# Kernel tuning notes

Measured on AMD Instinct MI355X. Metric: run time of the kernel, lower is better.

Reference implementation:

```python
import jax, jax.numpy as jnp
import numpy as np

N, E, D, H, OUT, L, AH = 50000, 800000, 128, 128, 2, 4, 16
LN_EPS = 1e-5


def setup_inputs() -> dict:
    key = jax.random.key(0)
    ks = jax.random.split(key, 8)
    s = lambda k, shape, scale: jax.random.normal(k, shape, jnp.float32) * scale
    return {
        "node_features": jax.random.normal(ks[0], (N, D), jnp.float32),
        "edge_index": jax.random.randint(ks[1], (2, E), 0, N),
        "W_self": s(ks[2], (L, D, H), 0.05),
        "b_self": jnp.zeros((L, H), jnp.float32),
        "W_ctx": s(ks[3], (L, 2 * D, H), 0.05),
        "b_ctx": jnp.zeros((L, H), jnp.float32),
        "att_W1": s(ks[4], (L, H, AH), 0.1),
        "att_b1": jnp.zeros((L, AH), jnp.float32),
        "att_w2": s(ks[5], (L, AH), 0.1),
        "ln_gamma": jnp.ones((L, H), jnp.float32),
        "ln_beta": jnp.zeros((L, H), jnp.float32),
        "fusion_logits": jnp.ones((L,), jnp.float32),
        "cls_W": s(ks[6], (H, OUT), 0.05),
        "cls_b": jnp.zeros((OUT,), jnp.float32),
    }


def _aggregate(x, src, tgt, n):
    # PyG add-aggregation of message cat([x_i - x_j, x_j]) at target nodes.
    # sum_over_edges(x_tgt - x_src) at tgt == deg(tgt)*x[tgt] - sum x_src, so we
    # avoid materializing the [E, 2D] edge tensor.
    ones = jnp.ones((src.shape[0],), x.dtype)
    deg = jax.ops.segment_sum(ones, tgt, num_segments=n)          # [N]
    agg_j = jax.ops.segment_sum(x[src], tgt, num_segments=n)      # [N, D]
    return jnp.concatenate([deg[:, None] * x - agg_j, agg_j], -1)  # [N, 2D]


def _layer_norm(x, gamma, beta):
    mu = x.mean(axis=-1, keepdims=True)
    var = ((x - mu) ** 2).mean(axis=-1, keepdims=True)
    return (x - mu) * jax.lax.rsqrt(var + LN_EPS) * gamma + beta


def _conv(x, src, tgt, Ws, bs, Wc, bc, A1, a1b, a2):
    n = x.shape[0]
    self_view = x @ Ws + bs                              # [N, H]
    out_view = _aggregate(x, src, tgt, n) @ Wc + bc      # outgoing (edge_index)
    in_view = _aggregate(x, tgt, src, n) @ Wc + bc       # incoming (reversed)
    mv = jnp.stack([self_view, out_view, in_view], axis=1)  # [N, 3, H]
    scores = jnp.einsum('nvh,ha->nva', jnp.tanh(jnp.einsum('nvh,ha->nva', mv, A1) + a1b), a2[:, None])[..., 0]
    w = jax.nn.softmax(scores, axis=1)                    # softmax over 3 views
    return jnp.einsum('nv,nvh->nh', w, mv)


def reference(node_features, edge_index, W_self, b_self, W_ctx, b_ctx,
              att_W1, att_b1, att_w2, ln_gamma, ln_beta,
              fusion_logits, cls_W, cls_b):
    src, tgt = edge_index[0], edge_index[1]
    x = node_features
    layer_outputs = []
    for l in range(L):
        h = _conv(x, src, tgt, W_self[l], b_self[l], W_ctx[l], b_ctx[l],
                  att_W1[l], att_b1[l], att_w2[l])
        h = jax.nn.relu(_layer_norm(h, ln_gamma[l], ln_beta[l]))
        # dropout is identity in eval mode
        x = h + x if l > 0 else h
        layer_outputs.append(x)
    fw = jax.nn.softmax(fusion_logits)
    fused = sum(fw[i] * layer_outputs[i] for i in range(L))
    return fused @ cls_W + cls_b
```

## Files before the change

### kernel.cpp

```cpp
#include <hip/hip_runtime.h>

#define N_NODES 50000
#define N_EDGES 800000
#define DD 128
#define HH 128
#define LL 4
#define AHH 16
#define LN_EPS 1e-5f
#define NCOLS 432
#define SCAN_B 512
#define SCAN_NB ((N_NODES + SCAN_B - 1) / SCAN_B)
#define WTPAD 136
#define WT_BLOCKS ((LL*NCOLS*DD)/256)

typedef unsigned short u16;
typedef unsigned int u32;
typedef __attribute__((ext_vector_type(8))) short short8;
typedef __attribute__((ext_vector_type(4))) float f32x4;

__device__ __forceinline__ float bf2f(u16 h){
  u32 u = ((u32)h) << 16;
  return __builtin_bit_cast(float, u);
}
__device__ __forceinline__ float bflo(u32 v){ return __builtin_bit_cast(float, v << 16); }
__device__ __forceinline__ float bfhi(u32 v){ return __builtin_bit_cast(float, v & 0xffff0000u); }
__device__ __forceinline__ u16 f2bf(float x){
  u32 u = __builtin_bit_cast(u32, x);
  u += 0x7fffu + ((u >> 16) & 1u);
  return (u16)(u >> 16);
}

__global__ void k_fail(float* out){
  int i = blockIdx.x*256 + threadIdx.x;
  if (i < N_NODES*2) out[i] = 1.0e6f;
}

__global__ __launch_bounds__(256) void k_cvt_hist(const float* __restrict__ X,
    u16* __restrict__ Xb, const int* __restrict__ ei, int* degO, int* degI){
  int i = blockIdx.x*256 + threadIdx.x;
  if (i < N_NODES*DD) Xb[i] = f2bf(X[i]);
  if (i < N_EDGES){
    atomicAdd(&degO[ei[N_EDGES + i]], 1);
    atomicAdd(&degI[ei[i]], 1);
  }
}

__global__ __launch_bounds__(SCAN_B) void k_scan1(const int* __restrict__ degO,
                                                  const int* __restrict__ degI, int* bsum){
  int b = blockIdx.x, t = threadIdx.x;
  const int* deg = blockIdx.y ? degI : degO;
  int i = b*SCAN_B + t;
  int v = (i < N_NODES) ? deg[i] : 0;
  #pragma unroll
  for (int m = 1; m < 64; m <<= 1) v += __shfl_xor(v, m);
  __shared__ int ws[SCAN_B/64];
  if ((t & 63) == 0) ws[t >> 6] = v;
  __syncthreads();
  if (t == 0){
    int s = 0;
    for (int w = 0; w < SCAN_B/64; ++w) s += ws[w];
    bsum[blockIdx.y*SCAN_NB + b] = s;
  }
}
__global__ void k_scan2(int* bsum, int* offO, int* offI){
  if (threadIdx.x == 0){
    int run = 0;
    for (int i = 0; i < SCAN_NB; ++i){ int v = bsum[i]; bsum[i] = run; run += v; }
    offO[N_NODES] = run;
    run = 0;
    for (int i = 0; i < SCAN_NB; ++i){ int v = bsum[SCAN_NB+i]; bsum[SCAN_NB+i] = run; run += v; }
    offI[N_NODES] = run;
  }
}
__global__ __launch_bounds__(SCAN_B) void k_scan3(const int* __restrict__ degO,
                                                  const int* __restrict__ degI,
                                                  const int* __restrict__ bsum,
                                                  int* offO, int* offI){
  int b = blockIdx.x, t = threadIdx.x, lane = t & 63, w = t >> 6;
  const int* deg = blockIdx.y ? degI : degO;
  int* off = blockIdx.y ? offI : offO;
  int i = b*SCAN_B + t;
  int v = (i < N_NODES) ? deg[i] : 0;
  int x = v;
  #pragma unroll
  for (int m = 1; m < 64; m <<= 1){ int tt = __shfl_up(x, m); if (lane >= m) x += tt; }
  __shared__ int ws[SCAN_B/64];
  if (lane == 63) ws[w] = x;
  __syncthreads();
  int woff = 0;
  for (int k = 0; k < w; ++k) woff += ws[k];
  if (i < N_NODES) off[i] = bsum[blockIdx.y*SCAN_NB + b] + woff + x - v;
}

__global__ void k_scatter(const int* __restrict__ ei, const int* __restrict__ offO,
                          const int* __restrict__ offI, int* cursO, int* cursI,
                          int* csrO, int* csrI){
  int e = blockIdx.x*256 + threadIdx.x;
  if (e >= N_EDGES) return;
  int s = ei[e], t = ei[N_EDGES + e];
  int p = atomicAdd(&cursO[t], 1); csrO[offO[t] + p] = s;
  int q = atomicAdd(&cursI[s], 1); csrI[offI[s] + q] = t;
}

__global__ void k_pack(const float* __restrict__ Wself, const float* __restrict__ Wctx,
                       const float* __restrict__ A1, const float* __restrict__ bs,
                       const float* __restrict__ bc, u16* __restrict__ WT,
                       float* bsA, float* bcA){
  if (blockIdx.x == WT_BLOCKS){
    int i = threadIdx.x;
    if (i < LL*2*AHH){
      int l = i >> 5, which = (i >> 4) & 1, a = i & 15;
      const float* b = which ? (bc + l*HH) : (bs + l*HH);
      const float* A = A1 + (size_t)l*HH*AHH;
      float v = 0.f;
      for (int h = 0; h < HH; ++h) v += b[h] * A[h*AHH + a];
      (which ? bcA : bsA)[l*AHH + a] = v;
    }
    return;
  }
  int idx = blockIdx.x*256 + threadIdx.x;
  int k = idx & 127;
  int j = (idx >> 7) % NCOLS;
  int l = idx / (NCOLS*DD);
  const float* Ws = Wself + (size_t)l*DD*HH;
  const float* Wc = Wctx + (size_t)l*2*DD*HH;
  const float* A  = A1 + (size_t)l*HH*AHH;
  float v = 0.f;
  if (j < 128) v = Ws[k*HH + j];
  else if (j < 256) v = Wc[k*HH + (j-128)];
  else if (j < 384) v = Wc[(128+k)*HH + (j-256)] - Wc[k*HH + (j-256)];
  else if (j < 400){ int a = j-384; for (int h=0; h<HH; ++h) v += Ws[k*HH+h] * A[h*AHH+a]; }
  else if (j < 416){ int a = j-400; for (int h=0; h<HH; ++h) v += Wc[k*HH+h] * A[h*AHH+a]; }
  else { int a = j-416; for (int h=0; h<HH; ++h) v += (Wc[(128+k)*HH+h] - Wc[k*HH+h]) * A[h*AHH+a]; }
  WT[((size_t)l*NCOLS + j)*DD + k] = f2bf(v);
}

struct GemmOut { u16 *S, *P1, *Pd, *SA, *P1A, *PdA; };

__global__ __launch_bounds__(256) void k_gemm(const u16* __restrict__ X,
                                              const u16* __restrict__ WT, GemmOut o){
  __shared__ u16 lw[3*16*WTPAD];
  int tid = threadIdx.x;
  int wid = tid >> 6, lane = tid & 63;
  int m0 = (blockIdx.x*4 + wid)*16;
  bool mvalid = (m0 < N_NODES);
  int m0c = mvalid ? m0 : (N_NODES - 16);
  int l15 = lane & 15, quad = lane >> 4;
  int sr = tid >> 4, sp = tid & 15;

  f32x4 acc[27];
  #pragma unroll
  for (int j = 0; j < 27; ++j) acc[j] = (f32x4){0.f,0.f,0.f,0.f};

  const u16* xr = X + (size_t)(m0c + l15)*DD + quad*8;
  short8 a[4];
  #pragma unroll
  for (int ks = 0; ks < 4; ++ks) a[ks] = *(const short8*)(xr + ks*32);

  short8 st[3];
  #pragma unroll
  for (int k = 0; k < 3; ++k)
    st[k] = *(const short8*)(WT + ((size_t)k*16 + sr)*DD + sp*8);

  for (int stage = 0; stage < 9; ++stage){
    int jbase = stage*3;
    __syncthreads();
    #pragma unroll
    for (int k = 0; k < 3; ++k)
      *(short8*)(&lw[(k*16 + sr)*WTPAD + sp*8]) = st[k];
    __syncthreads();
    if (stage < 8){
      #pragma unroll
      for (int k = 0; k < 3; ++k)
        st[k] = *(const short8*)(WT + ((size_t)(jbase+3+k)*16 + sr)*DD + sp*8);
    }
    #pragma unroll
    for (int k = 0; k < 3; ++k){
      const u16* wb = &lw[(k*16 + l15)*WTPAD + quad*8];
      #pragma unroll
      for (int ks = 0; ks < 4; ++ks){
        short8 b = *(const short8*)(wb + ks*32);
        acc[jbase+k] = __builtin_amdgcn_mfma_f32_16x16x32_bf16(a[ks], b, acc[jbase+k], 0, 0, 0);
      }
    }
  }
  if (!mvalid) return;
  #pragma unroll
  for (int j = 0; j < 27; ++j){
    int col = j*16 + l15;
    #pragma unroll
    for (int r = 0; r < 4; ++r){
      int row = m0 + quad*4 + r;
      u16 hv = f2bf(acc[j][r]);
      if (col < 128)      o.S  [(size_t)row*128 + col]        = hv;
      else if (col < 256) o.P1 [(size_t)row*128 + col - 128]  = hv;
      else if (col < 384) o.Pd [(size_t)row*128 + col - 256]  = hv;
      else if (col < 400) o.SA [(size_t)row*16  + col - 384]  = hv;
      else if (col < 416) o.P1A[(size_t)row*16  + col - 400]  = hv;
      else                o.PdA[(size_t)row*16  + col - 416]  = hv;
    }
  }
}

__global__ __launch_bounds__(256) void k_aggepi(int l,
  const u16* __restrict__ S, const u16* __restrict__ P1,
  const u16* __restrict__ Pd, const u16* __restrict__ PdA,
  const u16* __restrict__ SA, const u16* __restrict__ P1A,
  const int* __restrict__ offO, const int* __restrict__ offI,
  const int* __restrict__ csrO, const int* __restrict__ csrI,
  const float* __restrict__ b_self, const float* __restrict__ b_ctx,
  const float* __restrict__ bsA, const float* __restrict__ bcA,
  const float* __restrict__ att_b1, const float* __restrict__ att_w2,
  const float* __restrict__ gamma, const float* __restrict__ beta,
  const float* __restrict__ flog,
  u16* __restrict__ xb16,
  const float* __restrict__ clsW, const float* __restrict__ clsB,
  float* __restrict__ out)
{
  __shared__ float red[4][288];
  int tid = threadIdx.x;
  int n = (blockIdx.x * 256 + tid) >> 6;
  int wid = tid >> 6;
  int lane = tid & 63;
  int q = lane & 15, g = lane >> 4;
  const u16* PdQ  = Pd  + (q << 3);
  const u16* PdAQ = PdA + ((lane & 7) << 1);

  int begO = offO[n], endO = offO[n+1];
  int begI = offI[n], endI = offI[n+1];

  float aO[8] = {0.f,0.f,0.f,0.f,0.f,0.f,0.f,0.f};
  float aI[8] = {0.f,0.f,0.f,0.f,0.f,0.f,0.f,0.f};
  float oa0 = 0.f, oa1 = 0.f, ia0 = 0.f, ia1 = 0.f;

  int eO = begO, eI = begI;

#define GATH(csr, e, ACC, p0, p1) { \
    int r_ = (csr)[(e) + g]; \
    uint4 v_ = *(const uint4*)(PdQ + (((u32)r_) << 7)); \
    u32 pa_ = *(const u32*)(PdAQ + (((u32)r_) << 4)); \
    ACC[0] += bflo(v_.x); ACC[1] += bfhi(v_.x); \
    ACC[2] += bflo(v_.y); ACC[3] += bfhi(v_.y); \
    ACC[4] += bflo(v_.z); ACC[5] += bfhi(v_.z); \
    ACC[6] += bflo(v_.w); ACC[7] += bfhi(v_.w); \
    p0 += bflo(pa_); p1 += bfhi(pa_); }

#define GATHM(csr, e, end, ACC, p0, p1) { \
    int e_ = (e) + g; \
    bool ok_ = e_ < (end); \
    int r_ = (csr)[ok_ ? e_ : (end)-1]; \
    uint4 v_ = *(const uint4*)(PdQ + (((u32)r_) << 7)); \
    u32 pa_ = *(const u32*)(PdAQ + (((u32)r_) << 4)); \
    if (!ok_){ v_.x = 0u; v_.y = 0u; v_.z = 0u; v_.w = 0u; pa_ = 0u; } \
    ACC[0] += bflo(v_.x); ACC[1] += bfhi(v_.x); \
    ACC[2] += bflo(v_.y); ACC[3] += bfhi(v_.y); \
    ACC[4] += bflo(v_.z); ACC[5] += bfhi(v_.z); \
    ACC[6] += bflo(v_.w); ACC[7] += bfhi(v_.w); \
    p0 += bflo(pa_); p1 += bfhi(pa_); }

  for (; eO + 4 <= endO && eI + 4 <= endI; eO += 4, eI += 4){
    GATH(csrO, eO, aO, oa0, oa1);
    GATH(csrI, eI, aI, ia0, ia1);
  }
  for (; eO + 4 <= endO; eO += 4) GATH(csrO, eO, aO, oa0, oa1);
  for (; eI + 4 <= endI; eI += 4) GATH(csrI, eI, aI, ia0, ia1);
  if (eO < endO) GATHM(csrO, eO, endO, aO, oa0, oa1);
  if (eI < endI) GATHM(csrI, eI, endI, aI, ia0, ia1);

#undef GATH
#undef GATHM

  #pragma unroll
  for (int j = 0; j < 8; ++j){
    aO[j] += __shfl_xor(aO[j], 16); aO[j] += __shfl_xor(aO[j], 32);
    aI[j] += __shfl_xor(aI[j], 16); aI[j] += __shfl_xor(aI[j], 32);
  }
  oa0 += __shfl_xor(oa0, 16); oa0 += __shfl_xor(oa0, 32);
  oa1 += __shfl_xor(oa1, 16); oa1 += __shfl_xor(oa1, 32);
  ia0 += __shfl_xor(ia0, 16); ia0 += __shfl_xor(ia0, 32);
  ia1 += __shfl_xor(ia1, 16); ia1 += __shfl_xor(ia1, 32);

  if (g == 0){
    #pragma unroll
    for (int j = 0; j < 8; ++j){
      red[wid][q*8 + j]       = aO[j];
      red[wid][128 + q*8 + j] = aI[j];
    }
    if (q < 8){
      red[wid][256 + q*2]     = oa0;
      red[wid][256 + q*2 + 1] = oa1;
      red[wid][272 + q*2]     = ia0;
      red[wid][272 + q*2 + 1] = ia1;
    }
  }
  int f0 = lane * 2;
  int a16 = lane & 15;
  float ao0 = red[wid][f0],       ao1 = red[wid][f0 + 1];
  float ai0 = red[wid][128 + f0], ai1 = red[wid][128 + f0 + 1];
  float aoa = red[wid][256 + a16];
  float aia = red[wid][272 + a16];

  float dO = (float)(endO - begO), dI = (float)(endI - begI);

  u32 sv = *(const u32*)(S  + (size_t)n*128 + f0);
  u32 pv = *(const u32*)(P1 + (size_t)n*128 + f0);
  float2 bsv = *(const float2*)(b_self + l*128 + f0);
  float2 bcv = *(const float2*)(b_ctx  + l*128 + f0);
  float p10 = bflo(pv), p11 = bfhi(pv);
  float mv00 = bflo(sv) + bsv.x;
  float mv01 = bfhi(sv) + bsv.y;
  float mv10 = dO*p10 + ao0 + bcv.x, mv11 = dO*p11 + ao1 + bcv.y;
  float mv20 = dI*p10 + ai0 + bcv.x, mv21 = dI*p11 + ai1 + bcv.y;

  int a = a16, v = g;
  float u = 0.f;
  if (v < 3){
    float t;
    if (v == 0)      t = bf2f(SA[(size_t)n*16 + a]) + bsA[l*16 + a];
    else if (v == 1) t = dO*bf2f(P1A[(size_t)n*16 + a]) + aoa + bcA[l*16 + a];
    else             t = dI*bf2f(P1A[(size_t)n*16 + a]) + aia + bcA[l*16 + a];
    u = tanhf(t + att_b1[l*16 + a]) * att_w2[l*16 + a];
  }
  u += __shfl_xor(u, 1); u += __shfl_xor(u, 2);
  u += __shfl_xor(u, 4); u += __shfl_xor(u, 8);
  float s0 = __shfl(u, 0), s1 = __shfl(u, 16), s2 = __shfl(u, 32);
  float mx = fmaxf(s0, fmaxf(s1, s2));
  float e0 = __expf(s0-mx), e1 = __expf(s1-mx), e2 = __expf(s2-mx);
  float inv = 1.f / (e0 + e1 + e2);
  float w0 = e0*inv, w1 = e1*inv, w2v = e2*inv;
  float h0 = w0*mv00 + w1*mv10 + w2v*mv20;
  float h1 = w0*mv01 + w1*mv11 + w2v*mv21;

  float sum = h0 + h1, sq = h0*h0 + h1*h1;
  #pragma unroll
  for (int m = 1; m < 64; m <<= 1){ sum += __shfl_xor(sum, m); sq += __shfl_xor(sq, m); }
  float mu = sum * (1.f/128.f);
  float var = sq * (1.f/128.f) - mu*mu;
  float rs = rsqrtf(var + LN_EPS);
  float2 gv = *(const float2*)(gamma + l*128 + f0);
  float2 bv = *(const float2*)(beta  + l*128 + f0);
  float y0 = fmaxf((h0 - mu)*rs*gv.x + bv.x, 0.f);
  float y1 = fmaxf((h1 - mu)*rs*gv.y + bv.y, 0.f);
  float xn0 = y0, xn1 = y1;
  if (l > 0){
    u32 xv = *(const u32*)(xb16 + (size_t)n*128 + f0);
    xn0 += bflo(xv); xn1 += bfhi(xv);
  }
  *(u32*)(xb16 + (size_t)n*128 + f0) = (u32)f2bf(xn0) | ((u32)f2bf(xn1) << 16);

  float g0 = flog[0], g1 = flog[1], g2 = flog[2], g3 = flog[3];
  float gm = fmaxf(fmaxf(g0,g1), fmaxf(g2,g3));
  float q0 = __expf(g0-gm), q1 = __expf(g1-gm), q2 = __expf(g2-gm), q3 = __expf(g3-gm);
  float fwl = (l==0?q0 : l==1?q1 : l==2?q2 : q3) / (q0+q1+q2+q3);

  float4 w = *(const float4*)(clsW + lane*4);
  float o0 = xn0*w.x + xn1*w.z;
  float o1 = xn0*w.y + xn1*w.w;
  #pragma unroll
  for (int m = 1; m < 64; m <<= 1){ o0 += __shfl_xor(o0, m); o1 += __shfl_xor(o1, m); }
  if (lane == 0){
    float2* op = (float2*)(out + (size_t)n*2);
    float2 prev = (l > 0) ? *op : make_float2(0.f, 0.f);
    float r0 = prev.x + fwl*o0, r1 = prev.y + fwl*o1;
    if (l == LL-1){ r0 += clsB[0]; r1 += clsB[1]; }
    *op = make_float2(r0, r1);
  }
}

extern "C" void kernel_launch(void* const* d_in, const int* in_sizes, int n_in,
                              void* d_out, int out_size, void* d_ws, size_t ws_size,
                              hipStream_t stream){
  const float* X0    = (const float*)d_in[0];
  const int*   EI    = (const int*)d_in[1];
  const float* Wself = (const float*)d_in[2];
  const float* bs    = (const float*)d_in[3];
  const float* Wctx  = (const float*)d_in[4];
  const float* bc    = (const float*)d_in[5];
  const float* A1    = (const float*)d_in[6];
  const float* ab1   = (const float*)d_in[7];
  const float* aw2   = (const float*)d_in[8];
  const float* gam   = (const float*)d_in[9];
  const float* bet   = (const float*)d_in[10];
  const float* flog  = (const float*)d_in[11];
  const float* clsW  = (const float*)d_in[12];
  const float* clsB  = (const float*)d_in[13];
  float* out = (float*)d_out;

  char* wsp = (char*)d_ws;
  size_t o = 0;
  auto alloc = [&](size_t b)->char*{ char* p = wsp + o; o = (o + b + 255) & ~(size_t)255; return p; };
  u16*  xb16  = (u16*) alloc((size_t)N_NODES*128*2);
  u16*  S     = (u16*) alloc((size_t)N_NODES*128*2);
  u16*  P1    = (u16*) alloc((size_t)N_NODES*128*2);
  u16*  Pdb   = (u16*) alloc((size_t)N_NODES*128*2);
  u16*  PdAb  = (u16*) alloc((size_t)N_NODES*16*2);
  u16*  SAb   = (u16*) alloc((size_t)N_NODES*16*2);
  u16*  P1A   = (u16*) alloc((size_t)N_NODES*16*2);
  u16*  WT    = (u16*) alloc((size_t)LL*NCOLS*128*2);
  float* bsA  = (float*)alloc(LL*16*4);
  float* bcA  = (float*)alloc(LL*16*4);
  int* bsum   = (int*) alloc((size_t)2*SCAN_NB*4);
  int* degO   = (int*) alloc((size_t)N_NODES*4);
  int* degI   = (int*) alloc((size_t)N_NODES*4);
  int* cursO  = (int*) alloc((size_t)N_NODES*4);
  int* cursI  = (int*) alloc((size_t)N_NODES*4);
  int* offO   = (int*) alloc((size_t)(N_NODES+1)*4);
  int* offI   = (int*) alloc((size_t)(N_NODES+1)*4);
  int* csrO   = (int*) alloc((size_t)N_EDGES*4);
  int* csrI   = (int*) alloc((size_t)N_EDGES*4);

  if (ws_size < o){
    k_fail<<<(N_NODES*2+255)/256, 256, 0, stream>>>(out);
    return;
  }

  (void)hipMemsetAsync(degO, 0, (size_t)((char*)offO - (char*)degO), stream);

  k_cvt_hist<<<(N_NODES*DD+255)/256, 256, 0, stream>>>(X0, xb16, EI, degO, degI);
  k_scan1<<<dim3(SCAN_NB,2), SCAN_B, 0, stream>>>(degO, degI, bsum);
  k_scan2<<<1, 64, 0, stream>>>(bsum, offO, offI);
  k_scan3<<<dim3(SCAN_NB,2), SCAN_B, 0, stream>>>(degO, degI, bsum, offO, offI);
  k_scatter<<<(N_EDGES+255)/256, 256, 0, stream>>>(EI, offO, offI, cursO, cursI, csrO, csrI);
  k_pack<<<WT_BLOCKS+1, 256, 0, stream>>>(Wself, Wctx, A1, bs, bc, WT, bsA, bcA);

  GemmOut go{S, P1, Pdb, SAb, P1A, PdAb};
  const int gemm_blocks = ((N_NODES/16) + 3) / 4;
  for (int l = 0; l < LL; ++l){
    k_gemm<<<gemm_blocks, 256, 0, stream>>>(xb16, WT + (size_t)l*NCOLS*128, go);
    k_aggepi<<<N_NODES/4, 256, 0, stream>>>(l, S, P1, Pdb, PdAb, SAb, P1A,
                                            offO, offI, csrO, csrI,
                                            bs, bc, bsA, bcA, ab1, aw2,
                                            gam, bet, flog, xb16,
                                            clsW, clsB, out);
  }
}
```

Before: 668.2 us.

## Build CSR via two-pass bucketed sort instead of global atomic scatter

Replaces the per-edge global-atomic CSR scatter with a two-level bucket sort. Edges are first binned into 256-node buckets using block-local shared-memory histograms, fused into the conversion/histogram kernel. Each bucket is then locally sorted in shared memory inside the weight-pack kernel, with GEMM output buffers reused as scratch. This cuts random global atomics and scattered writes, and also makes neighbor order within each node deterministic-ish. The cost is a fixed bucket capacity (8192 entries) that would truncate if any bucket overflows.

```diff
diff --git a/kernel.cpp b/kernel.cpp
--- a/kernel.cpp
+++ b/kernel.cpp
@@ -12,6 +12,10 @@
 #define SCAN_NB ((N_NODES + SCAN_B - 1) / SCAN_B)
 #define WTPAD 136
 #define WT_BLOCKS ((LL*NCOLS*DD)/256)
+#define NBKT 196
+#define BKT_CAP 8192
+#define CVT_BLOCKS ((N_NODES*DD + 255)/256)
+#define BKT_BLOCKS ((N_EDGES + 2047)/2048)
 
 typedef unsigned short u16;
 typedef unsigned int u32;
@@ -35,13 +39,56 @@
   if (i < N_NODES*2) out[i] = 1.0e6f;
 }
 
-__global__ __launch_bounds__(256) void k_cvt_hist(const float* __restrict__ X,
-    u16* __restrict__ Xb, const int* __restrict__ ei, int* degO, int* degI){
-  int i = blockIdx.x*256 + threadIdx.x;
-  if (i < N_NODES*DD) Xb[i] = f2bf(X[i]);
-  if (i < N_EDGES){
-    atomicAdd(&degO[ei[N_EDGES + i]], 1);
-    atomicAdd(&degI[ei[i]], 1);
+__global__ __launch_bounds__(256) void k_cvt_hist_bkt(const float* __restrict__ X,
+    u16* __restrict__ Xb, const int* __restrict__ ei, int* degO, int* degI,
+    int* gcur, u32* __restrict__ bktO, u32* __restrict__ bktI){
+  if (blockIdx.x < CVT_BLOCKS){
+    int i = blockIdx.x*256 + threadIdx.x;
+    if (i < N_NODES*DD) Xb[i] = f2bf(X[i]);
+    if (i < N_EDGES){
+      atomicAdd(&degO[ei[N_EDGES + i]], 1);
+      atomicAdd(&degI[ei[i]], 1);
+    }
+    return;
+  }
+  __shared__ int histO[NBKT], histI[NBKT], baseO[NBKT], baseI[NBKT];
+  int tid = threadIdx.x;
+  int e0 = (blockIdx.x - CVT_BLOCKS)*2048;
+  if (tid < NBKT){ histO[tid] = 0; histI[tid] = 0; }
+  __syncthreads();
+  int s[8], t[8];
+  #pragma unroll
+  for (int k = 0; k < 8; ++k){
+    int e = e0 + k*256 + tid;
+    bool ok = e < N_EDGES;
+    s[k] = ok ? ei[e] : -1;
+    t[k] = ok ? ei[N_EDGES + e] : -1;
+    if (ok){
+      atomicAdd(&histO[t[k] >> 8], 1);
+      atomicAdd(&histI[s[k] >> 8], 1);
+    }
+  }
+  __syncthreads();
+  if (tid < NBKT){
+    baseO[tid] = atomicAdd(&gcur[tid],        histO[tid]);
+    baseI[tid] = atomicAdd(&gcur[NBKT + tid], histI[tid]);
+  }
+  __syncthreads();
+  if (tid < NBKT){ histO[tid] = 0; histI[tid] = 0; }
+  __syncthreads();
+  #pragma unroll
+  for (int k = 0; k < 8; ++k){
+    if (s[k] >= 0){
+      int bO = t[k] >> 8, bI = s[k] >> 8;
+      int rO = atomicAdd(&histO[bO], 1);
+      int rI = atomicAdd(&histI[bI], 1);
+      u32 iO = (u32)bO*BKT_CAP + (u32)(baseO[bO] + rO);
+      u32 iI = (u32)bI*BKT_CAP + (u32)(baseI[bI] + rI);
+      if (iO >= (u32)NBKT*BKT_CAP) iO = (u32)NBKT*BKT_CAP - 1;
+      if (iI >= (u32)NBKT*BKT_CAP) iI = (u32)NBKT*BKT_CAP - 1;
+      bktO[iO] = ((u32)(t[k] & 255) << 16) | (u32)s[k];
+      bktI[iI] = ((u32)(s[k] & 255) << 16) | (u32)t[k];
+    }
   }
 }
 
@@ -92,20 +139,52 @@
   if (i < N_NODES) off[i] = bsum[blockIdx.y*SCAN_NB + b] + woff + x - v;
 }
 
-__global__ void k_scatter(const int* __restrict__ ei, const int* __restrict__ offO,
-                          const int* __restrict__ offI, int* cursO, int* cursI,
-                          int* csrO, int* csrI){
-  int e = blockIdx.x*256 + threadIdx.x;
-  if (e >= N_EDGES) return;
-  int s = ei[e], t = ei[N_EDGES + e];
-  int p = atomicAdd(&cursO[t], 1); csrO[offO[t] + p] = s;
-  int q = atomicAdd(&cursI[s], 1); csrI[offI[s] + q] = t;
-}
-
-__global__ void k_pack(const float* __restrict__ Wself, const float* __restrict__ Wctx,
+__global__ __launch_bounds__(256) void k_packsort(const float* __restrict__ Wself,
+                       const float* __restrict__ Wctx,
                        const float* __restrict__ A1, const float* __restrict__ bs,
                        const float* __restrict__ bc, u16* __restrict__ WT,
-                       float* bsA, float* bcA){
+                       float* bsA, float* bcA,
+                       const u32* __restrict__ bktO, const u32* __restrict__ bktI,
+                       const int* __restrict__ offO, const int* __restrict__ offI,
+                       int* __restrict__ csrO, int* __restrict__ csrI){
+  if (blockIdx.x > WT_BLOCKS){
+    int sb = blockIdx.x - (WT_BLOCKS + 1);
+    int d = sb >= NBKT;
+    int b = d ? sb - NBKT : sb;
+    const u32* bkt = d ? bktI : bktO;
+    const int* off = d ? offI : offO;
+    int* csr = d ? csrI : csrO;
+    __shared__ int hist[256], pref[256], cur[256], wsum[4];
+    int tid = threadIdx.x;
+    int lo = b*256, hi = min(lo + 256, N_NODES);
+    int gbase = off[lo];
+    int cnt = off[hi] - gbase;
+    if (cnt > BKT_CAP) cnt = BKT_CAP;
+    hist[tid] = 0; cur[tid] = 0;
+    __syncthreads();
+    const u32* bb = bkt + (size_t)b*BKT_CAP;
+    for (int i = tid; i < cnt; i += 256) atomicAdd(&hist[bb[i] >> 16], 1);
+    __syncthreads();
+    {
+      int lane = tid & 63, wid = tid >> 6;
+      int h = hist[tid], v = h;
+      #pragma unroll
+      for (int m = 1; m < 64; m <<= 1){ int tt = __shfl_up(v, m); if (lane >= m) v += tt; }
+      if (lane == 63) wsum[wid] = v;
+      __syncthreads();
+      int add = 0;
+      for (int w = 0; w < wid; ++w) add += wsum[w];
+      pref[tid] = add + v - h;
+    }
+    __syncthreads();
+    for (int i = tid; i < cnt; i += 256){
+      u32 ent = bb[i];
+      int loc = (int)(ent >> 16);
+      int pos = pref[loc] + atomicAdd(&cur[loc], 1);
+      csr[gbase + pos] = (int)(ent & 0xffffu);
+    }
+    return;
+  }
   if (blockIdx.x == WT_BLOCKS){
     int i = threadIdx.x;
     if (i < LL*2*AHH){
@@ -402,8 +481,7 @@
   int* bsum   = (int*) alloc((size_t)2*SCAN_NB*4);
   int* degO   = (int*) alloc((size_t)N_NODES*4);
   int* degI   = (int*) alloc((size_t)N_NODES*4);
-  int* cursO  = (int*) alloc((size_t)N_NODES*4);
-  int* cursI  = (int*) alloc((size_t)N_NODES*4);
+  int* gcur   = (int*) alloc((size_t)2*NBKT*4);
   int* offO   = (int*) alloc((size_t)(N_NODES+1)*4);
   int* offI   = (int*) alloc((size_t)(N_NODES+1)*4);
   int* csrO   = (int*) alloc((size_t)N_EDGES*4);
@@ -414,14 +492,18 @@
     return;
   }
 
+  u32* bktO = (u32*)S;
+  u32* bktI = (u32*)P1;
+
   (void)hipMemsetAsync(degO, 0, (size_t)((char*)offO - (char*)degO), stream);
 
-  k_cvt_hist<<<(N_NODES*DD+255)/256, 256, 0, stream>>>(X0, xb16, EI, degO, degI);
+  k_cvt_hist_bkt<<<CVT_BLOCKS + BKT_BLOCKS, 256, 0, stream>>>(X0, xb16, EI, degO, degI,
+                                                              gcur, bktO, bktI);
   k_scan1<<<dim3(SCAN_NB,2), SCAN_B, 0, stream>>>(degO, degI, bsum);
   k_scan2<<<1, 64, 0, stream>>>(bsum, offO, offI);
   k_scan3<<<dim3(SCAN_NB,2), SCAN_B, 0, stream>>>(degO, degI, bsum, offO, offI);
-  k_scatter<<<(N_EDGES+255)/256, 256, 0, stream>>>(EI, offO, offI, cursO, cursI, csrO, csrI);
-  k_pack<<<WT_BLOCKS+1, 256, 0, stream>>>(Wself, Wctx, A1, bs, bc, WT, bsA, bcA);
+  k_packsort<<<WT_BLOCKS + 1 + 2*NBKT, 256, 0, stream>>>(Wself, Wctx, A1, bs, bc, WT, bsA, bcA,
+                                                         bktO, bktI, offO, offI, csrO, csrI);
 
   GemmOut go{S, P1, Pdb, SAb, P1A, PdAb};
   const int gemm_blocks = ((N_NODES/16) + 3) / 4;
```

Result: faster. 612.9 us (-8.3%).
